# Kernel optimization log

Measured on AMD Instinct MI355X. Metric: run time of the kernel, lower is better.

Reference implementation:

```python
import jax, jax.numpy as jnp
import numpy as np

H = 512

def _lstm_cell(x, h, c, Wih, Whh, bih, bhh):
    # torch LSTM gate order: i, f, g, o
    g = x @ Wih.T + bih + h @ Whh.T + bhh  # (B, 4H)
    i, f, gg, o = jnp.split(g, 4, axis=-1)
    i = jax.nn.sigmoid(i); f = jax.nn.sigmoid(f)
    gg = jnp.tanh(gg);     o = jax.nn.sigmoid(o)
    c_new = f * c + i * gg
    h_new = o * jnp.tanh(c_new)
    return h_new, c_new

def setup_inputs() -> dict:
    key = jax.random.key(0)
    ks = jax.random.split(key, 16)
    B, S, F = 32, 128, 2
    s = 1.0 / np.sqrt(H)
    u = lambda k, shape: jax.random.uniform(k, shape, jnp.float32, -s, s)
    return {
        "inputs": jax.random.normal(ks[0], (B, S, F), jnp.float32),
        "Wp": u(ks[1], (H, F)), "bp": u(ks[2], (H,)),
        "enc_Wih": u(ks[3], (4 * H, H)), "enc_Whh": u(ks[4], (4 * H, H)),
        "enc_bih": u(ks[5], (4 * H,)),   "enc_bhh": u(ks[6], (4 * H,)),
        "dec_Wih": u(ks[7], (4 * H, H)), "dec_Whh": u(ks[8], (4 * H, H)),
        "dec_bih": u(ks[9], (4 * H,)),   "dec_bhh": u(ks[10], (4 * H,)),
        "W1": u(ks[11], (H, H)), "W2": u(ks[12], (H, H)),
        "v": u(ks[13], (H,)),
    }

def reference(inputs, Wp, bp, enc_Wih, enc_Whh, enc_bih, enc_bhh,
              dec_Wih, dec_Whh, dec_bih, dec_bhh, W1, W2, v):
    B, S, _ = inputs.shape
    trg_len = S
    x = inputs @ Wp.T + bp  # (B, S, H) input projection

    # --- encoder LSTM over time ---
    h0 = jnp.zeros((B, H), inputs.dtype)
    c0 = jnp.zeros((B, H), inputs.dtype)
    def enc_step(carry, xt):
        h, c = carry
        h, c = _lstm_cell(xt, h, c, enc_Wih, enc_Whh, enc_bih, enc_bhh)
        return (h, c), h
    (h, c), enc_hs = jax.lax.scan(enc_step, (h0, c0), jnp.swapaxes(x, 0, 1))
    encoder_outputs = jnp.swapaxes(enc_hs, 0, 1)  # (B, S, H)

    # loop-invariant encoder projection (hoisted; identical math)
    enc_proj = encoder_outputs @ W1.T  # (B, S, H)

    # NOTE: the original module never updates its mask (stays all-False),
    # so masking is a no-op and is faithfully omitted.
    dec_in0 = jnp.zeros((B, H), inputs.dtype)
    batch_idx = jnp.arange(B)

    def dec_step(carry, _):
        h, c, dec_in = carry
        h, c = _lstm_cell(dec_in, h, c, dec_Wih, dec_Whh, dec_bih, dec_bhh)
        dec_proj = h @ W2.T  # (B, H)
        scores = jnp.einsum('bsh,h->bs', jnp.tanh(enc_proj + dec_proj[:, None, :]), v)
        log_probs = jax.nn.log_softmax(scores, axis=-1)  # (B, S)
        top_idx = jnp.argmax(log_probs, axis=-1)  # (B,)
        next_in = encoder_outputs[batch_idx, top_idx]  # (B, H)
        return (h, c, next_in), log_probs

    _, all_lp = jax.lax.scan(dec_step, (h, c, dec_in0), None, length=trg_len)
    return jnp.swapaxes(all_lp, 0, 1)  # (B, trg_len, S)
```

## Files before the change

### kernel.cpp

```cpp
#include <hip/hip_runtime.h>
#include <math.h>

static constexpr int H   = 512;
static constexpr int B   = 32;
static constexpr int S   = 128;
static constexpr int G4  = 2048;
static constexpr int UPS = 64;
static constexpr int RPS = 256;
static constexpr int NSL = 8;

static constexpr size_t OFF_E   = 0;
static constexpr size_t SZ_E    = (size_t)B * S * G4;
static constexpr size_t OFF_EO  = OFF_E + SZ_E;
static constexpr size_t SZ_EO   = (size_t)B * S * H;
static constexpr size_t OFF_PT  = OFF_EO + SZ_EO;
static constexpr size_t SZ_PT   = (size_t)B * H * S;
static constexpr size_t OFF_WPE = OFF_PT + SZ_PT;
static constexpr size_t SZ_WP   = (size_t)NSL * H * RPS;
static constexpr size_t OFF_WPD = OFF_WPE + SZ_WP;
static constexpr size_t OFF_W2T = OFF_WPD + SZ_WP;
static constexpr size_t OFF_HB  = OFF_W2T + (size_t)H * H;
static constexpr size_t OFF_CB  = OFF_HB + (size_t)B * 2 * H;
static constexpr size_t OFF_PS  = OFF_CB + (size_t)B * H;
static constexpr size_t OFF_M1  = OFF_PS + (size_t)B * 2 * 512;
static constexpr size_t OFF_BE  = OFF_M1 + (size_t)G4 * 2;
static constexpr size_t OFF_DB  = OFF_BE + G4;
static constexpr size_t OFF_END = OFF_DB + G4;
static constexpr int CTRL_U32 = (256 + 256 + 128 + 32) * 32;

__device__ __forceinline__ float sigm(float x){
  float e = __expf(-x);
  return 1.0f / (1.0f + e);
}
__device__ __forceinline__ float tanh_(float x){
  float e = __expf(2.0f * x);
  return 1.0f - 2.0f / (1.0f + e);
}

__device__ __forceinline__ float cloadf(const float* p){
  union { unsigned u; float f; } c;
  c.u = __hip_atomic_load((const unsigned*)p, __ATOMIC_RELAXED,
                          __HIP_MEMORY_SCOPE_AGENT);
  return c.f;
}
__device__ __forceinline__ float2 cload2(const float* p){
  union { unsigned long long u; float2 f; } c;
  c.u = __hip_atomic_load((const unsigned long long*)p, __ATOMIC_RELAXED,
                          __HIP_MEMORY_SCOPE_AGENT);
  return c.f;
}
__device__ __forceinline__ void cstore2(float* p, float a, float b){
  union { unsigned long long u; float2 f; } c;
  c.f = make_float2(a, b);
  __hip_atomic_store((unsigned long long*)p, c.u, __ATOMIC_RELAXED,
                     __HIP_MEMORY_SCOPE_AGENT);
}
__device__ __forceinline__ unsigned cloadu(const unsigned* p){
  return __hip_atomic_load(p, __ATOMIC_RELAXED, __HIP_MEMORY_SCOPE_AGENT);
}
__device__ __forceinline__ void cstoreu(unsigned* p, unsigned v){
  __hip_atomic_store(p, v, __ATOMIC_RELAXED, __HIP_MEMORY_SCOPE_AGENT);
}

__global__ __launch_bounds__(256) void prep_misc(
    const float* __restrict__ eWih, const float* __restrict__ Wp,
    const float* __restrict__ bp,  const float* __restrict__ ebih,
    const float* __restrict__ ebhh, const float* __restrict__ dbih,
    const float* __restrict__ dbhh,
    float* __restrict__ M1, float* __restrict__ bias_e, float* __restrict__ dbias)
{
  int c = blockIdx.x * 256 + threadIdx.x;
  const float* wr = eWih + (size_t)c * H;
  float m0 = 0.f, m1 = 0.f, mb = 0.f;
  for (int k = 0; k < H; k += 4){
    float4 w  = *(const float4*)(wr + k);
    float4 p0 = *(const float4*)(Wp + (size_t)k * 2);
    float4 p1 = *(const float4*)(Wp + (size_t)(k + 2) * 2);
    float4 bb = *(const float4*)(bp + k);
    m0 += w.x*p0.x + w.y*p0.z + w.z*p1.x + w.w*p1.z;
    m1 += w.x*p0.y + w.y*p0.w + w.z*p1.y + w.w*p1.w;
    mb += w.x*bb.x + w.y*bb.y + w.z*bb.z + w.w*bb.w;
  }
  M1[(size_t)c*2]   = m0;
  M1[(size_t)c*2+1] = m1;
  bias_e[c] = ebih[c] + ebhh[c] + mb;
  dbias[c]  = dbih[c] + dbhh[c];
}

__global__ __launch_bounds__(256) void efill(
    const float* __restrict__ inp, const float* __restrict__ M1,
    const float* __restrict__ be, float* __restrict__ E)
{
  size_t i = (size_t)blockIdx.x * 256 + threadIdx.x;
  int c = (int)(i & 2047);
  int t = (int)((i >> 11) & 127);
  int b = (int)(i >> 18);
  float x0 = inp[((size_t)b * S + t) * 2 + 0];
  float x1 = inp[((size_t)b * S + t) * 2 + 1];
  E[i] = M1[(size_t)c*2] * x0 + M1[(size_t)c*2+1] * x1 + be[c];
}

__global__ __launch_bounds__(256) void pack_whh(
    const float* __restrict__ Whh, float* __restrict__ WP)
{
  size_t i = (size_t)blockIdx.x * 256 + threadIdx.x;
  int p = (int)(i & 255);
  int k = (int)((i >> 8) & 511);
  int j = (int)(i >> 17);
  int g = p >> 6, u = p & 63;
  int r = g * 512 + j * UPS + u;
  WP[i] = Whh[(size_t)r * H + k];
}

__global__ __launch_bounds__(256) void transpose_k(
    const float* __restrict__ in, float* __restrict__ out, int R, int K)
{
  __shared__ float tile[32][33];
  int r0 = blockIdx.y * 32, k0 = blockIdx.x * 32;
  int tx = threadIdx.x & 31, ty = threadIdx.x >> 5;
  #pragma unroll
  for (int j = 0; j < 4; ++j)
    tile[ty + 8*j][tx] = in[(size_t)(r0 + ty + 8*j) * K + k0 + tx];
  __syncthreads();
  #pragma unroll
  for (int j = 0; j < 4; ++j)
    out[(size_t)(k0 + ty + 8*j) * R + r0 + tx] = tile[tx][ty + 8*j];
}

template<int LAYOUT>
__global__ __launch_bounds__(256) void gemm_nt(
    const float* __restrict__ A, const float* __restrict__ Bm,
    const float* __restrict__ bias, float* __restrict__ C,
    int M, int N, int K)
{
  __shared__ float As[16][68];
  __shared__ float Bs[16][68];
  int tid = threadIdx.x;
  int bm = blockIdx.y * 64, bn = blockIdx.x * 64;
  int tm = (tid & 15) * 4, tn = (tid >> 4) * 4;
  float acc[4][4] = {};
  int r  = tid >> 2;
  int kq = (tid & 3) * 4;
  for (int k0 = 0; k0 < K; k0 += 16){
    float4 a = *(const float4*)(A  + (size_t)(bm + r) * K + k0 + kq);
    float4 b = *(const float4*)(Bm + (size_t)(bn + r) * K + k0 + kq);
    __syncthreads();
    As[kq+0][r] = a.x; As[kq+1][r] = a.y; As[kq+2][r] = a.z; As[kq+3][r] = a.w;
    Bs[kq+0][r] = b.x; Bs[kq+1][r] = b.y; Bs[kq+2][r] = b.z; Bs[kq+3][r] = b.w;
    __syncthreads();
    #pragma unroll
    for (int kk = 0; kk < 16; ++kk){
      float4 av = *(const float4*)(&As[kk][tm]);
      float4 bv = *(const float4*)(&Bs[kk][tn]);
      acc[0][0] += av.x*bv.x; acc[0][1] += av.x*bv.y; acc[0][2] += av.x*bv.z; acc[0][3] += av.x*bv.w;
      acc[1][0] += av.y*bv.x; acc[1][1] += av.y*bv.y; acc[1][2] += av.y*bv.z; acc[1][3] += av.y*bv.w;
      acc[2][0] += av.z*bv.x; acc[2][1] += av.z*bv.y; acc[2][2] += av.z*bv.z; acc[2][3] += av.z*bv.w;
      acc[3][0] += av.w*bv.x; acc[3][1] += av.w*bv.y; acc[3][2] += av.w*bv.z; acc[3][3] += av.w*bv.w;
    }
  }
  #pragma unroll
  for (int i = 0; i < 4; ++i){
    int m = bm + tm + i;
    #pragma unroll
    for (int j = 0; j < 4; ++j){
      int n = bn + tn + j;
      float vv = acc[i][j] + (bias ? bias[n] : 0.f);
      if (LAYOUT == 0) C[(size_t)m * N + n] = vv;
      else             C[((size_t)(m >> 7) * 512 + n) * 128 + (m & 127)] = vv;
    }
  }
}

__global__ __launch_bounds__(256) void encoder_kernel(
    const float* __restrict__ WP,
    const float* __restrict__ E,
    float* __restrict__ hb,
    float* __restrict__ c_buf,
    float* __restrict__ enc_out,
    unsigned* __restrict__ htags)
{
  __shared__ float hsh[H];
  __shared__ float gpart[4][RPS];
  __shared__ float gfin[4][UPS];
  __shared__ float hloc[UPS];
  const int tid = threadIdx.x, bk = blockIdx.x;
  const int b = bk >> 3, j = bk & 7;
  const int u0 = j * UPS;
  const float* wp = WP + (size_t)j * H * RPS;
  unsigned* myhtags = htags + (size_t)b * 8 * 32;
  const int ph = tid >> 6, c4 = tid & 63;
  float creg = 0.f;
  for (int t = 0; t < S; ++t){
    if (t > 0 && tid < 8){
      while (cloadu(myhtags + tid * 32) < (unsigned)t){}
    }
    __syncthreads();
    { float2 q = cload2(hb + ((size_t)b * 2 + ((t + 1) & 1)) * H + 2 * tid);
      hsh[2*tid] = q.x; hsh[2*tid + 1] = q.y; }
    __syncthreads();
    float4 acc = {0.f, 0.f, 0.f, 0.f};
    const float* wq = wp + ph * RPS + c4 * 4;
    #pragma unroll 4
    for (int kk = 0; kk < 128; ++kk){
      float hv = hsh[4*kk + ph];
      float4 w = *(const float4*)(wq + (size_t)kk * 4 * RPS);
      acc.x = fmaf(w.x, hv, acc.x); acc.y = fmaf(w.y, hv, acc.y);
      acc.z = fmaf(w.z, hv, acc.z); acc.w = fmaf(w.w, hv, acc.w);
    }
    *(float4*)&gpart[ph][c4 * 4] = acc;
    __syncthreads();
    if (tid < 64){
      float4 s0 = *(const float4*)&gpart[0][tid*4];
      float4 s1 = *(const float4*)&gpart[1][tid*4];
      float4 s2 = *(const float4*)&gpart[2][tid*4];
      float4 s3 = *(const float4*)&gpart[3][tid*4];
      int g = tid >> 4, uu = (tid & 15) * 4;
      float4 e = *(const float4*)(E + ((size_t)b * S + t) * G4 + g * 512 + u0 + uu);
      float4 s; s.x = s0.x+s1.x+s2.x+s3.x + e.x; s.y = s0.y+s1.y+s2.y+s3.y + e.y;
      s.z = s0.z+s1.z+s2.z+s3.z + e.z; s.w = s0.w+s1.w+s2.w+s3.w + e.w;
      *(float4*)&gfin[g][uu] = s;
    }
    __syncthreads();
    if (tid < UPS){
      float gi = gfin[0][tid], gf = gfin[1][tid], gg = gfin[2][tid], go = gfin[3][tid];
      creg = sigm(gf) * creg + sigm(gi) * tanh_(gg);
      hloc[tid] = sigm(go) * tanh_(creg);
    }
    __syncthreads();
    if (tid < 32){
      float h0 = hloc[2*tid], h1 = hloc[2*tid + 1];
      cstore2(hb + ((size_t)b * 2 + (t & 1)) * H + u0 + 2*tid, h0, h1);
      *(float2*)(enc_out + ((size_t)b * S + t) * H + u0 + 2*tid) = make_float2(h0, h1);
    }
    __syncthreads();
    if (tid == 0) cstoreu(myhtags + j * 32, (unsigned)(t + 1));
  }
  if (tid < UPS) c_buf[(size_t)b * H + u0 + tid] = creg;
}

__global__ __launch_bounds__(256) void decoder_kernel(
    const float* __restrict__ WP,
    const float* __restrict__ D,
    const float* __restrict__ dbias,
    const float* __restrict__ W2T,
    const float* __restrict__ Pt,
    const float* __restrict__ vvec,
    const float* __restrict__ c_buf,
    const float* __restrict__ enc_out,
    float* __restrict__ hb,
    float* __restrict__ psbuf,
    unsigned* __restrict__ htags,
    unsigned* __restrict__ pstags,
    unsigned* __restrict__ otags,
    float* __restrict__ out)
{
  const int tid = threadIdx.x, bk = blockIdx.x;
  if (bk < 256){
    __shared__ float hsh[H];
    __shared__ float gpart[4][RPS];
    __shared__ float gfin[4][UPS];
    __shared__ float hloc[UPS];
    __shared__ float wm[2]; __shared__ int wi[2];
    const int b = bk >> 3, j = bk & 7;
    const int u0 = j * UPS;
    const float* wp = WP + (size_t)j * H * RPS;
    unsigned* myhtags = htags + (size_t)b * 8 * 32;
    const int ph = tid >> 6, c4 = tid & 63;
    float creg = (tid < UPS) ? c_buf[(size_t)b * H + u0 + tid] : 0.f;
    if (tid < 32){
      float2 hv = *(const float2*)(enc_out + ((size_t)b * S + (S-1)) * H + u0 + 2*tid);
      cstore2(hb + ((size_t)b * 2 + 1) * H + u0 + 2*tid, hv.x, hv.y);
    }
    __syncthreads();
    if (tid == 0) cstoreu(myhtags + j * 32, 1u);
    for (int t = 0; t < S; ++t){
      if (tid < 8){
        while (cloadu(myhtags + tid * 32) < (unsigned)(t + 1)) __builtin_amdgcn_s_sleep(1);
      }
      __syncthreads();
      { float2 q = cload2(hb + ((size_t)b * 2 + ((t + 1) & 1)) * H + 2 * tid);
        hsh[2*tid] = q.x; hsh[2*tid + 1] = q.y; }
      __syncthreads();
      float4 acc = {0.f, 0.f, 0.f, 0.f};
      const float* wq = wp + ph * RPS + c4 * 4;
      #pragma unroll 4
      for (int kk = 0; kk < 128; ++kk){
        float hv = hsh[4*kk + ph];
        float4 w = *(const float4*)(wq + (size_t)kk * 4 * RPS);
        acc.x = fmaf(w.x, hv, acc.x); acc.y = fmaf(w.y, hv, acc.y);
        acc.z = fmaf(w.z, hv, acc.z); acc.w = fmaf(w.w, hv, acc.w);
      }
      *(float4*)&gpart[ph][c4 * 4] = acc;
      if (t >= 1 && tid < 4){
        while (cloadu(pstags + (size_t)(b * 4 + tid) * 32) < (unsigned)t)
          __builtin_amdgcn_s_sleep(1);
      }
      __syncthreads();
      if (t >= 1 && tid < 128){
        const float* pp = psbuf + ((size_t)b * 2 + ((t + 1) & 1)) * 512 + tid;
        float sc = cloadf(pp) + cloadf(pp + 128) + cloadf(pp + 256) + cloadf(pp + 384);
        float mv = sc; int mi = tid;
        #pragma unroll
        for (int off = 32; off > 0; off >>= 1){
          float ov = __shfl_xor(mv, off, 64);
          int   oi = __shfl_xor(mi, off, 64);
          if (ov > mv || (ov == mv && oi < mi)){ mv = ov; mi = oi; }
        }
        if ((tid & 63) == 0){ wm[tid >> 6] = mv; wi[tid >> 6] = mi; }
      }
      __syncthreads();
      int top = 0;
      if (t >= 1)
        top = (wm[1] > wm[0] || (wm[1] == wm[0] && wi[1] < wi[0])) ? wi[1] : wi[0];
      if (tid < 64){
        float4 s0 = *(const float4*)&gpart[0][tid*4];
        float4 s1 = *(const float4*)&gpart[1][tid*4];
        float4 s2 = *(const float4*)&gpart[2][tid*4];
        float4 s3 = *(const float4*)&gpart[3][tid*4];
        int g = tid >> 4, uu = (tid & 15) * 4;
        const float* xr = (t == 0) ? dbias : D + ((size_t)b * S + top) * G4;
        float4 e = *(const float4*)(xr + g * 512 + u0 + uu);
        float4 s; s.x = s0.x+s1.x+s2.x+s3.x + e.x; s.y = s0.y+s1.y+s2.y+s3.y + e.y;
        s.z = s0.z+s1.z+s2.z+s3.z + e.z; s.w = s0.w+s1.w+s2.w+s3.w + e.w;
        *(float4*)&gfin[g][uu] = s;
      }
      __syncthreads();
      if (tid < UPS){
        float gi = gfin[0][tid], gf = gfin[1][tid], gg = gfin[2][tid], go = gfin[3][tid];
        creg = sigm(gf) * creg + sigm(gi) * tanh_(gg);
        hloc[tid] = sigm(go) * tanh_(creg);
      }
      __syncthreads();
      if (tid < 32)
        cstore2(hb + ((size_t)b * 2 + (t & 1)) * H + u0 + 2*tid,
                hloc[2*tid], hloc[2*tid + 1]);
      __syncthreads();
      if (tid == 0) cstoreu(myhtags + j * 32, (unsigned)(t + 2));
    }
  } else if (bk < 384){
    __shared__ float hsh[H];
    __shared__ float dps[2][128];
    __shared__ float dpl[128];
    __shared__ float vsh2[128];
    __shared__ float pspart[2][128];
    const int b = (bk - 256) >> 2, q = (bk - 256) & 3;
    const unsigned* myhtags = htags + (size_t)b * 8 * 32;
    unsigned* mytag = pstags + (size_t)(b * 4 + q) * 32;
    const unsigned* myotag = otags + (size_t)b * 32;
    if (tid < 128) vsh2[tid] = vvec[q * 128 + tid];
    for (int tau = 0; tau < S; ++tau){
      if (tid < 8){
        while (cloadu(myhtags + tid * 32) < (unsigned)(tau + 2)) __builtin_amdgcn_s_sleep(1);
      } else if (tid == 8 && tau >= 2){
        while (cloadu(myotag) < (unsigned)(tau - 1)) __builtin_amdgcn_s_sleep(1);
      }
      __syncthreads();
      { float2 qq = cload2(hb + ((size_t)b * 2 + (tau & 1)) * H + 2 * tid);
        hsh[2*tid] = qq.x; hsh[2*tid + 1] = qq.y; }
      __syncthreads();
      {
        int nl = tid & 127, kh = tid >> 7;
        const float* w = W2T + (size_t)(kh * 256) * H + q * 128 + nl;
        float a = 0.f;
        #pragma unroll 8
        for (int k2 = 0; k2 < 256; ++k2)
          a = fmaf(w[(size_t)k2 * H], hsh[kh * 256 + k2], a);
        dps[kh][nl] = a;
      }
      __syncthreads();
      if (tid < 128) dpl[tid] = dps[0][tid] + dps[1][tid];
      __syncthreads();
      {
        int s = tid & 127, nh = tid >> 7;
        const float* Pp = Pt + ((size_t)b * H + q * 128 + nh * 64) * S + s;
        float cs = 0.f;
        #pragma unroll 4
        for (int n = 0; n < 64; ++n){
          float x = Pp[(size_t)n * S] + dpl[nh * 64 + n];
          cs = fmaf(vsh2[nh * 64 + n], tanh_(x), cs);
        }
        pspart[nh][s] = cs;
      }
      __syncthreads();
      if (tid < 64)
        cstore2(psbuf + ((size_t)b * 2 + (tau & 1)) * 512 + q * 128 + 2 * tid,
                pspart[0][2*tid] + pspart[1][2*tid],
                pspart[0][2*tid+1] + pspart[1][2*tid+1]);
      __syncthreads();
      if (tid == 0) cstoreu(mytag, (unsigned)(tau + 1));
    }
  } else {
    __shared__ float wm2[2]; __shared__ float wsum[2];
    const int b = bk - 384;
    unsigned* myotag = otags + (size_t)b * 32;
    for (int t = 0; t < S; ++t){
      if (tid < 4){
        while (cloadu(pstags + (size_t)(b * 4 + tid) * 32) < (unsigned)(t + 1))
          __builtin_amdgcn_s_sleep(1);
      }
      __syncthreads();
      float sc = 0.f;
      if (tid < 128){
        const float* pp = psbuf + ((size_t)b * 2 + (t & 1)) * 512 + tid;
        sc = cloadf(pp) + cloadf(pp + 128) + cloadf(pp + 256) + cloadf(pp + 384);
        float mv = sc;
        #pragma unroll
        for (int off = 32; off > 0; off >>= 1)
          mv = fmaxf(mv, __shfl_xor(mv, off, 64));
        if ((tid & 63) == 0) wm2[tid >> 6] = mv;
      }
      __syncthreads();
      float mglob = fmaxf(wm2[0], wm2[1]);
      if (tid < 128){
        float ss = __expf(sc - mglob);
        #pragma unroll
        for (int off = 32; off > 0; off >>= 1) ss += __shfl_xor(ss, off, 64);
        if ((tid & 63) == 0) wsum[tid >> 6] = ss;
      }
      __syncthreads();
      if (tid < 128){
        float lse = __logf(wsum[0] + wsum[1]);
        out[((size_t)b * S + t) * S + tid] = sc - mglob - lse;
      }
      __syncthreads();
      if (tid == 0) cstoreu(myotag, (unsigned)(t + 1));
    }
  }
}

extern "C" void kernel_launch(void* const* d_in, const int* in_sizes, int n_in,
                              void* d_out, int out_size, void* d_ws, size_t ws_size,
                              hipStream_t stream) {
  const float* inputs  = (const float*)d_in[0];
  const float* Wp      = (const float*)d_in[1];
  const float* bp      = (const float*)d_in[2];
  const float* eWih    = (const float*)d_in[3];
  const float* eWhh    = (const float*)d_in[4];
  const float* ebih    = (const float*)d_in[5];
  const float* ebhh    = (const float*)d_in[6];
  const float* dWih    = (const float*)d_in[7];
  const float* dWhh    = (const float*)d_in[8];
  const float* dbih    = (const float*)d_in[9];
  const float* dbhh    = (const float*)d_in[10];
  const float* W1      = (const float*)d_in[11];
  const float* W2      = (const float*)d_in[12];
  const float* v       = (const float*)d_in[13];
  float* out = (float*)d_out;

  float* ws = (float*)d_ws;
  float* E       = ws + OFF_E;
  float* enc_out = ws + OFF_EO;
  float* Pt      = ws + OFF_PT;
  float* WPe     = ws + OFF_WPE;
  float* WPd     = ws + OFF_WPD;
  float* W2T     = ws + OFF_W2T;
  float* hb      = ws + OFF_HB;
  float* c_buf   = ws + OFF_CB;
  float* psbuf   = ws + OFF_PS;
  float* M1      = ws + OFF_M1;
  float* bias_e  = ws + OFF_BE;
  float* dbias   = ws + OFF_DB;
  unsigned* enc_htags = (unsigned*)(ws + OFF_END);
  unsigned* dec_htags = enc_htags + 256 * 32;
  unsigned* pstags    = dec_htags + 256 * 32;
  unsigned* otags     = pstags + 128 * 32;

  hipMemsetAsync(hb, 0, (size_t)B * 2 * H * sizeof(float), stream);
  hipMemsetAsync(enc_htags, 0, CTRL_U32 * sizeof(unsigned), stream);

  prep_misc<<<G4 / 256, 256, 0, stream>>>(eWih, Wp, bp, ebih, ebhh, dbih, dbhh,
                                          M1, bias_e, dbias);
  efill<<<(int)(SZ_E / 256), 256, 0, stream>>>(inputs, M1, bias_e, E);
  pack_whh<<<(int)(SZ_WP / 256), 256, 0, stream>>>(eWhh, WPe);
  pack_whh<<<(int)(SZ_WP / 256), 256, 0, stream>>>(dWhh, WPd);
  { dim3 g(H / 32, H / 32); transpose_k<<<g, 256, 0, stream>>>(W2, W2T, H, H); }

  encoder_kernel<<<256, 256, 0, stream>>>(WPe, E, hb, c_buf, enc_out, enc_htags);

  float* D = E;
  { dim3 grid(G4 / 64, (B * S) / 64);
    gemm_nt<0><<<grid, 256, 0, stream>>>(enc_out, dWih, dbias, D, B * S, G4, H); }
  { dim3 grid(H / 64, (B * S) / 64);
    gemm_nt<1><<<grid, 256, 0, stream>>>(enc_out, W1, nullptr, Pt, B * S, H, H); }

  decoder_kernel<<<416, 256, 0, stream>>>(WPd, D, dbias, W2T, Pt, v, c_buf,
                                          enc_out, hb, psbuf,
                                          dec_htags, pstags, otags, out);
  (void)in_sizes; (void)n_in; (void)out_size; (void)ws_size;
}
```

Measured before the change: 2.933 ms.

## Fuse attention score blocks into decoder LSTM blocks, splitting scores across 8 slices

Removes the separate 128 attention-score blocks and has each of the 8 LSTM slice blocks per batch compute the W2 projection and the tanh/v partial scores for its own 64 hidden units, publishing 8 partials per batch. This cuts the grid from 416 to 288 blocks and drops one cross-block handoff (LSTM to score blocks) from the recurrent critical path. In exchange, the score work now runs serially inside the recurrent LSTM blocks each step, and the argmax/softmax readers must sum 8 partials instead of 4.

```diff
diff --git a/kernel.cpp b/kernel.cpp
--- a/kernel.cpp
+++ b/kernel.cpp
@@ -22,11 +22,12 @@
 static constexpr size_t OFF_HB  = OFF_W2T + (size_t)H * H;
 static constexpr size_t OFF_CB  = OFF_HB + (size_t)B * 2 * H;
 static constexpr size_t OFF_PS  = OFF_CB + (size_t)B * H;
-static constexpr size_t OFF_M1  = OFF_PS + (size_t)B * 2 * 512;
+static constexpr size_t SZ_PS   = (size_t)B * 2 * 8 * 128;
+static constexpr size_t OFF_M1  = OFF_PS + SZ_PS;
 static constexpr size_t OFF_BE  = OFF_M1 + (size_t)G4 * 2;
 static constexpr size_t OFF_DB  = OFF_BE + G4;
 static constexpr size_t OFF_END = OFF_DB + G4;
-static constexpr int CTRL_U32 = (256 + 256 + 128 + 32) * 32;
+static constexpr int CTRL_U32 = (256 + 256 + 256 + 32) * 32;
 
 __device__ __forceinline__ float sigm(float x){
   float e = __expf(-x);
@@ -260,13 +261,20 @@
     __shared__ float gpart[4][RPS];
     __shared__ float gfin[4][UPS];
     __shared__ float hloc[UPS];
+    __shared__ float dps[4][UPS];
+    __shared__ float dpl[UPS];
+    __shared__ float vsh[UPS];
+    __shared__ float pspart[2][128];
     __shared__ float wm[2]; __shared__ int wi[2];
     const int b = bk >> 3, j = bk & 7;
     const int u0 = j * UPS;
     const float* wp = WP + (size_t)j * H * RPS;
-    unsigned* myhtags = htags + (size_t)b * 8 * 32;
+    unsigned* myhtags  = htags  + (size_t)b * 8 * 32;
+    unsigned* mypstags = pstags + (size_t)b * 8 * 32;
+    const unsigned* myotag = otags + (size_t)b * 32;
     const int ph = tid >> 6, c4 = tid & 63;
     float creg = (tid < UPS) ? c_buf[(size_t)b * H + u0 + tid] : 0.f;
+    if (tid < UPS) vsh[tid] = vvec[u0 + tid];
     if (tid < 32){
       float2 hv = *(const float2*)(enc_out + ((size_t)b * S + (S-1)) * H + u0 + 2*tid);
       cstore2(hb + ((size_t)b * 2 + 1) * H + u0 + 2*tid, hv.x, hv.y);
@@ -276,11 +284,45 @@
     for (int t = 0; t < S; ++t){
       if (tid < 8){
         while (cloadu(myhtags + tid * 32) < (unsigned)(t + 1)) __builtin_amdgcn_s_sleep(1);
+      } else if (tid == 8 && t >= 3){
+        while (cloadu(myotag) < (unsigned)(t - 2)) __builtin_amdgcn_s_sleep(1);
       }
       __syncthreads();
       { float2 q = cload2(hb + ((size_t)b * 2 + ((t + 1) & 1)) * H + 2 * tid);
         hsh[2*tid] = q.x; hsh[2*tid + 1] = q.y; }
       __syncthreads();
+      if (t >= 1){
+        {
+          int nl = tid & 63, kq = tid >> 6;
+          const float* w = W2T + (size_t)(kq * 128) * H + u0 + nl;
+          float a = 0.f;
+          #pragma unroll 8
+          for (int k2 = 0; k2 < 128; ++k2)
+            a = fmaf(w[(size_t)k2 * H], hsh[kq * 128 + k2], a);
+          dps[kq][nl] = a;
+        }
+        __syncthreads();
+        if (tid < UPS) dpl[tid] = dps[0][tid] + dps[1][tid] + dps[2][tid] + dps[3][tid];
+        __syncthreads();
+        {
+          int s = tid & 127, nh = tid >> 7;
+          const float* Pp = Pt + ((size_t)b * H + u0 + nh * 32) * S + s;
+          float cs = 0.f;
+          #pragma unroll 4
+          for (int n = 0; n < 32; ++n){
+            float x = Pp[(size_t)n * S] + dpl[nh * 32 + n];
+            cs = fmaf(vsh[nh * 32 + n], tanh_(x), cs);
+          }
+          pspart[nh][s] = cs;
+        }
+        __syncthreads();
+        if (tid < 64)
+          cstore2(psbuf + (((size_t)b * 2 + ((t - 1) & 1)) * 8 + j) * 128 + 2 * tid,
+                  pspart[0][2*tid] + pspart[1][2*tid],
+                  pspart[0][2*tid+1] + pspart[1][2*tid+1]);
+        __syncthreads();
+        if (tid == 0) cstoreu(mypstags + j * 32, (unsigned)t);
+      }
       float4 acc = {0.f, 0.f, 0.f, 0.f};
       const float* wq = wp + ph * RPS + c4 * 4;
       #pragma unroll 4
@@ -291,14 +333,15 @@
         acc.z = fmaf(w.z, hv, acc.z); acc.w = fmaf(w.w, hv, acc.w);
       }
       *(float4*)&gpart[ph][c4 * 4] = acc;
-      if (t >= 1 && tid < 4){
-        while (cloadu(pstags + (size_t)(b * 4 + tid) * 32) < (unsigned)t)
-          __builtin_amdgcn_s_sleep(1);
+      if (t >= 1 && tid < 8){
+        while (cloadu(mypstags + tid * 32) < (unsigned)t) __builtin_amdgcn_s_sleep(1);
       }
       __syncthreads();
       if (t >= 1 && tid < 128){
-        const float* pp = psbuf + ((size_t)b * 2 + ((t + 1) & 1)) * 512 + tid;
-        float sc = cloadf(pp) + cloadf(pp + 128) + cloadf(pp + 256) + cloadf(pp + 384);
+        const float* pp = psbuf + ((size_t)b * 2 + ((t - 1) & 1)) * 8 * 128 + tid;
+        float sc = 0.f;
+        #pragma unroll
+        for (int jj2 = 0; jj2 < 8; ++jj2) sc += cloadf(pp + jj2 * 128);
         float mv = sc; int mi = tid;
         #pragma unroll
         for (int off = 32; off > 0; off >>= 1){
@@ -337,72 +380,61 @@
       __syncthreads();
       if (tid == 0) cstoreu(myhtags + j * 32, (unsigned)(t + 2));
     }
-  } else if (bk < 384){
-    __shared__ float hsh[H];
-    __shared__ float dps[2][128];
-    __shared__ float dpl[128];
-    __shared__ float vsh2[128];
-    __shared__ float pspart[2][128];
-    const int b = (bk - 256) >> 2, q = (bk - 256) & 3;
-    const unsigned* myhtags = htags + (size_t)b * 8 * 32;
-    unsigned* mytag = pstags + (size_t)(b * 4 + q) * 32;
-    const unsigned* myotag = otags + (size_t)b * 32;
-    if (tid < 128) vsh2[tid] = vvec[q * 128 + tid];
-    for (int tau = 0; tau < S; ++tau){
-      if (tid < 8){
-        while (cloadu(myhtags + tid * 32) < (unsigned)(tau + 2)) __builtin_amdgcn_s_sleep(1);
-      } else if (tid == 8 && tau >= 2){
-        while (cloadu(myotag) < (unsigned)(tau - 1)) __builtin_amdgcn_s_sleep(1);
-      }
-      __syncthreads();
-      { float2 qq = cload2(hb + ((size_t)b * 2 + (tau & 1)) * H + 2 * tid);
-        hsh[2*tid] = qq.x; hsh[2*tid + 1] = qq.y; }
-      __syncthreads();
-      {
-        int nl = tid & 127, kh = tid >> 7;
-        const float* w = W2T + (size_t)(kh * 256) * H + q * 128 + nl;
-        float a = 0.f;
-        #pragma unroll 8
-        for (int k2 = 0; k2 < 256; ++k2)
-          a = fmaf(w[(size_t)k2 * H], hsh[kh * 256 + k2], a);
-        dps[kh][nl] = a;
-      }
-      __syncthreads();
-      if (tid < 128) dpl[tid] = dps[0][tid] + dps[1][tid];
-      __syncthreads();
-      {
-        int s = tid & 127, nh = tid >> 7;
-        const float* Pp = Pt + ((size_t)b * H + q * 128 + nh * 64) * S + s;
-        float cs = 0.f;
-        #pragma unroll 4
-        for (int n = 0; n < 64; ++n){
-          float x = Pp[(size_t)n * S] + dpl[nh * 64 + n];
-          cs = fmaf(vsh2[nh * 64 + n], tanh_(x), cs);
-        }
-        pspart[nh][s] = cs;
-      }
-      __syncthreads();
-      if (tid < 64)
-        cstore2(psbuf + ((size_t)b * 2 + (tau & 1)) * 512 + q * 128 + 2 * tid,
-                pspart[0][2*tid] + pspart[1][2*tid],
-                pspart[0][2*tid+1] + pspart[1][2*tid+1]);
-      __syncthreads();
-      if (tid == 0) cstoreu(mytag, (unsigned)(tau + 1));
-    }
+    if (tid < 8){
+      while (cloadu(myhtags + tid * 32) < (unsigned)(S + 1)) __builtin_amdgcn_s_sleep(1);
+    } else if (tid == 8){
+      while (cloadu(myotag) < (unsigned)(S - 2)) __builtin_amdgcn_s_sleep(1);
+    }
+    __syncthreads();
+    { float2 q = cload2(hb + ((size_t)b * 2 + 1) * H + 2 * tid);
+      hsh[2*tid] = q.x; hsh[2*tid + 1] = q.y; }
+    __syncthreads();
+    {
+      int nl = tid & 63, kq = tid >> 6;
+      const float* w = W2T + (size_t)(kq * 128) * H + u0 + nl;
+      float a = 0.f;
+      #pragma unroll 8
+      for (int k2 = 0; k2 < 128; ++k2)
+        a = fmaf(w[(size_t)k2 * H], hsh[kq * 128 + k2], a);
+      dps[kq][nl] = a;
+    }
+    __syncthreads();
+    if (tid < UPS) dpl[tid] = dps[0][tid] + dps[1][tid] + dps[2][tid] + dps[3][tid];
+    __syncthreads();
+    {
+      int s = tid & 127, nh = tid >> 7;
+      const float* Pp = Pt + ((size_t)b * H + u0 + nh * 32) * S + s;
+      float cs = 0.f;
+      #pragma unroll 4
+      for (int n = 0; n < 32; ++n){
+        float x = Pp[(size_t)n * S] + dpl[nh * 32 + n];
+        cs = fmaf(vsh[nh * 32 + n], tanh_(x), cs);
+      }
+      pspart[nh][s] = cs;
+    }
+    __syncthreads();
+    if (tid < 64)
+      cstore2(psbuf + (((size_t)b * 2 + ((S - 1) & 1)) * 8 + j) * 128 + 2 * tid,
+              pspart[0][2*tid] + pspart[1][2*tid],
+              pspart[0][2*tid+1] + pspart[1][2*tid+1]);
+    __syncthreads();
+    if (tid == 0) cstoreu(mypstags + j * 32, (unsigned)S);
   } else {
     __shared__ float wm2[2]; __shared__ float wsum[2];
-    const int b = bk - 384;
+    const int b = bk - 256;
     unsigned* myotag = otags + (size_t)b * 32;
+    const unsigned* mypstags = pstags + (size_t)b * 8 * 32;
     for (int t = 0; t < S; ++t){
-      if (tid < 4){
-        while (cloadu(pstags + (size_t)(b * 4 + tid) * 32) < (unsigned)(t + 1))
+      if (tid < 8){
+        while (cloadu(mypstags + tid * 32) < (unsigned)(t + 1))
           __builtin_amdgcn_s_sleep(1);
       }
       __syncthreads();
       float sc = 0.f;
       if (tid < 128){
-        const float* pp = psbuf + ((size_t)b * 2 + (t & 1)) * 512 + tid;
-        sc = cloadf(pp) + cloadf(pp + 128) + cloadf(pp + 256) + cloadf(pp + 384);
+        const float* pp = psbuf + ((size_t)b * 2 + (t & 1)) * 8 * 128 + tid;
+        #pragma unroll
+        for (int jj2 = 0; jj2 < 8; ++jj2) sc += cloadf(pp + jj2 * 128);
         float mv = sc;
         #pragma unroll
         for (int off = 32; off > 0; off >>= 1)
@@ -463,7 +495,7 @@
   unsigned* enc_htags = (unsigned*)(ws + OFF_END);
   unsigned* dec_htags = enc_htags + 256 * 32;
   unsigned* pstags    = dec_htags + 256 * 32;
-  unsigned* otags     = pstags + 128 * 32;
+  unsigned* otags     = pstags + 256 * 32;
 
   hipMemsetAsync(hb, 0, (size_t)B * 2 * H * sizeof(float), stream);
   hipMemsetAsync(enc_htags, 0, CTRL_U32 * sizeof(unsigned), stream);
@@ -483,7 +515,7 @@
   { dim3 grid(H / 64, (B * S) / 64);
     gemm_nt<1><<<grid, 256, 0, stream>>>(enc_out, W1, nullptr, Pt, B * S, H, H); }
 
-  decoder_kernel<<<416, 256, 0, stream>>>(WPd, D, dbias, W2T, Pt, v, c_buf,
+  decoder_kernel<<<288, 256, 0, stream>>>(WPd, D, dbias, W2T, Pt, v, c_buf,
                                           enc_out, hb, psbuf,
                                           dec_htags, pstags, otags, out);
   (void)in_sizes; (void)n_in; (void)out_size; (void)ws_size;
```

New measurement: 3.001 ms. 1.02x slower.
